# Performance work log

Hardware: AMD Instinct MI355X
Metric: run time of the kernel (lower is better)

Reference implementation:

```python
import jax, jax.numpy as jnp
import numpy as np

B, T, DIN, DC, CS = 8, 4096, 1024, 256, 8192
EPS = 1e-12

def _l2norm(x):
    # F.normalize: x / max(||x||_2, eps) along last axis
    n = jnp.sqrt(jnp.sum(x * x, axis=-1, keepdims=True))
    return x / jnp.maximum(n, EPS)

def _wn(v, g):
    # torch weight_norm(dim=0): w = g * v / ||v|| per output row
    n = jnp.sqrt(jnp.sum(v * v, axis=1, keepdims=True))
    return g * v / jnp.maximum(n, EPS)

def setup_inputs() -> dict:
    key = jax.random.key(0)
    k = jax.random.split(key, 4)
    return {
        "z": jax.random.normal(k[0], (B, DIN, T), jnp.float32),
        "in_v": jax.random.normal(k[1], (DC, DIN), jnp.float32) * 0.02,
        "in_g": jnp.ones((DC, 1), jnp.float32),
        "in_b": jnp.zeros((DC,), jnp.float32),
        "out_v": jax.random.normal(k[2], (DIN, DC), jnp.float32) * 0.02,
        "out_g": jnp.ones((DIN, 1), jnp.float32),
        "out_b": jnp.zeros((DIN,), jnp.float32),
        "codebook": jax.random.normal(k[3], (CS, DC), jnp.float32),
    }

def reference(z, in_v, in_g, in_b, out_v, out_g, out_b, codebook):
    b, _, t = z.shape
    w_in = _wn(in_v, in_g)                      # (DC, DIN)
    z_e = jnp.einsum('bdt,cd->bct', z, w_in) + in_b[None, :, None]  # (B, DC, T)

    # decode_latents (eval mode: dropout p=0)
    enc = _l2norm(z_e.transpose(0, 2, 1).reshape(b * t, -1))   # (BT, DC)
    cb = _l2norm(codebook)                                     # (CS, DC)
    dist = (jnp.sum(enc * enc, axis=1, keepdims=True)
            - 2.0 * enc @ cb.T
            + jnp.sum(cb * cb, axis=1)[None, :])               # (BT, CS)
    indices = jnp.argmax(-dist, axis=1).reshape(b, t)          # (B, T)
    z_q = codebook[indices].transpose(0, 2, 1)                 # (B, DC, T)

    commitment_loss = jnp.mean((z_e - jax.lax.stop_gradient(z_q)) ** 2, axis=(1, 2))
    codebook_loss = jnp.mean((z_q - jax.lax.stop_gradient(z_e)) ** 2, axis=(1, 2))

    z_q_st = z_e + jax.lax.stop_gradient(z_q - z_e)            # straight-through
    w_out = _wn(out_v, out_g)                                  # (DIN, DC)
    z_q_out = jnp.einsum('bct,dc->bdt', z_q_st, w_out) + out_b[None, :, None]
    return (z_q_out, commitment_loss, codebook_loss, indices)
```

## Files before the change

### kernel.cpp

```cpp
#include <hip/hip_runtime.h>
#include <stdint.h>

#define BB 8
#define TT 4096
#define DIN 1024
#define DC 256
#define CS 8192
#define EPSF 1e-12f

typedef unsigned short ushort_t;
typedef __attribute__((ext_vector_type(8))) short short8;
typedef __attribute__((ext_vector_type(4))) float f32x4;

constexpr size_t OFF_WIN   = 0;
constexpr size_t OFF_WOUTT = OFF_WIN   + 1048576;
constexpr size_t OFF_CBN   = OFF_WOUTT + 1048576;
constexpr size_t OFF_NRM2  = OFF_CBN   + 8388608;
constexpr size_t OFF_ZE    = OFF_NRM2  + 32768;
constexpr size_t OFF_INV   = OFF_ZE    + 33554432;
constexpr size_t OFF_ENC2  = OFF_INV   + 131072;
constexpr size_t OFF_KEYS  = OFF_ENC2  + 131072;
constexpr size_t OFF_LOSS  = OFF_KEYS  + 262144;
constexpr size_t OFF_WSPL  = OFF_LOSS  + 256;
constexpr size_t OFF_W2T   = OFF_WSPL  + 1048576;
constexpr size_t REQ_WS_ZE = OFF_W2T + 134217728ull;

__device__ __forceinline__ float block_reduce_sum_256(float v, float* sbuf) {
  #pragma unroll
  for (int o = 32; o > 0; o >>= 1) v += __shfl_down(v, o, 64);
  int lane = threadIdx.x & 63, w = threadIdx.x >> 6;
  if (lane == 0) sbuf[w] = v;
  __syncthreads();
  float r = sbuf[0] + sbuf[1] + sbuf[2] + sbuf[3];
  __syncthreads();
  return r;
}

__device__ __forceinline__ ushort_t bf16_rne(float x) {
  unsigned u = __float_as_uint(x);
  unsigned r = (u + 0x7FFFu + ((u >> 16) & 1u)) >> 16;
  return (ushort_t)r;
}
__device__ __forceinline__ float bf16f(ushort_t h) {
  return __uint_as_float(((unsigned)h) << 16);
}

__device__ __forceinline__ int swz4(int r) {
  return (r + (r >> 2)) & 3;
}

__device__ __forceinline__ void async_copy16(const ushort_t* g, ushort_t* lds) {
  __builtin_amdgcn_global_load_lds(
      (const __attribute__((address_space(1))) void*)g,
      (__attribute__((address_space(3))) void*)lds, 16, 0, 0);
}

__device__ __forceinline__ void stage_tile8(const ushort_t* __restrict__ s0,
                                            ushort_t* __restrict__ dstbuf,
                                            const int (&go)[8]) {
  #pragma unroll
  for (int i = 0; i < 8; i++) async_copy16(s0 + go[i], dstbuf + i*512);
}

__device__ __forceinline__ void stage2(const ushort_t* __restrict__ srcbase,
                                       ushort_t* __restrict__ comp,
                                       const int (&go)[2], int wu) {
  async_copy16(srcbase + go[0], comp + wu);
  async_copy16(srcbase + go[1], comp + wu + 4096);
}

#define LD8(base, off) (*(const short8*)((const char*)(base) + (off)))

template<int MH, int CLO>
__device__ __forceinline__ void qmfma(f32x4 (&acc)[8][4],
    const short8 (&fah)[4], const short8 (&fal)[4],
    const short8 (&fbh)[4], const short8 (&fbl)[4]) {
  #pragma unroll
  for (int r = 0; r < 4; r++) {
    #pragma unroll
    for (int c2 = 0; c2 < 2; c2++) {
      f32x4 t = acc[MH*4 + r][CLO + c2];
      t = __builtin_amdgcn_mfma_f32_16x16x32_bf16(fah[r], fbh[CLO + c2], t, 0, 0, 0);
      t = __builtin_amdgcn_mfma_f32_16x16x32_bf16(fal[r], fbh[CLO + c2], t, 0, 0, 0);
      t = __builtin_amdgcn_mfma_f32_16x16x32_bf16(fah[r], fbl[CLO + c2], t, 0, 0, 0);
      acc[MH*4 + r][CLO + c2] = t;
    }
  }
}

__global__ void k_prep_win(const float* __restrict__ v, const float* __restrict__ g,
                           float* __restrict__ w, ushort_t* __restrict__ wh,
                           ushort_t* __restrict__ wl) {
  __shared__ float sb[4];
  int r = blockIdx.x, t = threadIdx.x;
  float xv[4]; float s = 0.f;
  #pragma unroll
  for (int i = 0; i < 4; i++) { xv[i] = v[r*DIN + t + i*256]; s += xv[i]*xv[i]; }
  s = block_reduce_sum_256(s, sb);
  float sc = g[r] / fmaxf(sqrtf(s), EPSF);
  #pragma unroll
  for (int i = 0; i < 4; i++) {
    float val = xv[i] * sc;
    int idx = r*DIN + t + i*256;
    w[idx] = val;
    ushort_t h = bf16_rne(val);
    wh[idx] = h;
    wl[idx] = bf16_rne(val - bf16f(h));
  }
}

__global__ void k_prep_wout(const float* __restrict__ v, const float* __restrict__ g,
                            float* __restrict__ wT) {
  __shared__ float sb[4];
  int r = blockIdx.x, t = threadIdx.x;
  float x = v[r*DC + t];
  float s = block_reduce_sum_256(x*x, sb);
  float sc = g[r] / fmaxf(sqrtf(s), EPSF);
  wT[t*DIN + r] = x * sc;
}

__global__ void k_prep_cb(const float* __restrict__ cb, ushort_t* __restrict__ cbh,
                          ushort_t* __restrict__ cbl, float* __restrict__ nrm2) {
  __shared__ float sb[4];
  int j = blockIdx.x, t = threadIdx.x;
  float x = cb[j*DC + t];
  float s = block_reduce_sum_256(x*x, sb);
  float nm = fmaxf(sqrtf(s), EPSF);
  float cn = x / nm;
  ushort_t h = bf16_rne(cn);
  cbh[j*DC + t] = h;
  cbl[j*DC + t] = bf16_rne(cn - bf16f(h));
  float q = block_reduce_sum_256(cn*cn, sb);
  if (t == 0) nrm2[j] = q;
}

__global__ void k_split_cbraw(const float* __restrict__ cb, ushort_t* __restrict__ ch,
                              ushort_t* __restrict__ cl) {
  int j = blockIdx.x, t = threadIdx.x;
  float x = cb[j*DC + t];
  ushort_t h = bf16_rne(x);
  ch[j*DC + t] = h;
  cl[j*DC + t] = bf16_rne(x - bf16f(h));
}

__global__ void k_split_wout(const float* __restrict__ v, const float* __restrict__ g,
                             ushort_t* __restrict__ wh, ushort_t* __restrict__ wl) {
  __shared__ float sb[4];
  int r = blockIdx.x, t = threadIdx.x;
  float x = v[r*DC + t];
  float s = block_reduce_sum_256(x*x, sb);
  float sc = g[r] / fmaxf(sqrtf(s), EPSF);
  float val = x * sc;
  ushort_t h = bf16_rne(val);
  wh[r*DC + t] = h;
  wl[r*DC + t] = bf16_rne(val - bf16f(h));
}

template<bool BIAS>
__global__ __launch_bounds__(256) void k_gemm(
    const float* __restrict__ A, const float* __restrict__ Bmat,
    const float* __restrict__ bias, float* __restrict__ C,
    int K, int lda, int ldb, int ldc, size_t strideB, size_t strideC)
{
  __shared__ float As[16][132];
  __shared__ float Bs[16][132];
  const int bn = blockIdx.x * 128;
  const int bm = blockIdx.y * 128;
  const float* Bb = Bmat + (size_t)blockIdx.z * strideB;
  float* Cb = C + (size_t)blockIdx.z * strideC;
  const int tid = threadIdx.x;
  const int tx = tid & 15, ty = tid >> 4;
  const int am = tid & 127, akq = (tid >> 7) * 8;
  const int bk = tid >> 5, bj = (tid & 31) * 4;

  float acc[8][8];
  #pragma unroll
  for (int i = 0; i < 8; i++)
    #pragma unroll
    for (int j = 0; j < 8; j++) acc[i][j] = 0.f;

  for (int k0 = 0; k0 < K; k0 += 16) {
    float4 a0 = *(const float4*)&A[(size_t)(bm+am)*lda + k0 + akq];
    float4 a1 = *(const float4*)&A[(size_t)(bm+am)*lda + k0 + akq + 4];
    float4 b0 = *(const float4*)&Bb[(size_t)(k0+bk)*ldb + bn + bj];
    float4 b1 = *(const float4*)&Bb[(size_t)(k0+bk+8)*ldb + bn + bj];
    As[akq+0][am] = a0.x; As[akq+1][am] = a0.y; As[akq+2][am] = a0.z; As[akq+3][am] = a0.w;
    As[akq+4][am] = a1.x; As[akq+5][am] = a1.y; As[akq+6][am] = a1.z; As[akq+7][am] = a1.w;
    *(float4*)&Bs[bk][bj] = b0;
    *(float4*)&Bs[bk+8][bj] = b1;
    __syncthreads();
    #pragma unroll
    for (int k = 0; k < 16; k++) {
      float av[8], bv[8];
      float4 x0 = *(const float4*)&As[k][tx*4];
      float4 x1 = *(const float4*)&As[k][tx*4+64];
      float4 y0 = *(const float4*)&Bs[k][ty*4];
      float4 y1 = *(const float4*)&Bs[k][ty*4+64];
      av[0]=x0.x; av[1]=x0.y; av[2]=x0.z; av[3]=x0.w;
      av[4]=x1.x; av[5]=x1.y; av[6]=x1.z; av[7]=x1.w;
      bv[0]=y0.x; bv[1]=y0.y; bv[2]=y0.z; bv[3]=y0.w;
      bv[4]=y1.x; bv[5]=y1.y; bv[6]=y1.z; bv[7]=y1.w;
      #pragma unroll
      for (int i = 0; i < 8; i++)
        #pragma unroll
        for (int j = 0; j < 8; j++)
          acc[i][j] += av[i] * bv[j];
    }
    __syncthreads();
  }

  #pragma unroll
  for (int i = 0; i < 8; i++) {
    int mm = bm + ((i < 4) ? tx*4 + i : 64 + tx*4 + (i-4));
    float bia = BIAS ? bias[mm] : 0.f;
    float4 v0 = make_float4(acc[i][0]+bia, acc[i][1]+bia, acc[i][2]+bia, acc[i][3]+bia);
    float4 v1 = make_float4(acc[i][4]+bia, acc[i][5]+bia, acc[i][6]+bia, acc[i][7]+bia);
    *(float4*)&Cb[(size_t)mm*ldc + bn + ty*4]      = v0;
    *(float4*)&Cb[(size_t)mm*ldc + bn + 64 + ty*4] = v1;
  }
}

__global__ void k_split_z(const float* __restrict__ z, ushort_t* __restrict__ zhi,
                          ushort_t* __restrict__ zlo) {
  __shared__ float tile[64][65];
  int b = blockIdx.z, t0 = blockIdx.x * 64, d0 = blockIdx.y * 64;
  int tx = threadIdx.x & 63, ty = threadIdx.x >> 6;
  const float* zb = z + (size_t)b*DIN*TT;
  #pragma unroll
  for (int i = 0; i < 16; i++) {
    int d = i*4 + ty;
    tile[d][tx] = zb[(size_t)(d0+d)*TT + t0 + tx];
  }
  __syncthreads();
  #pragma unroll
  for (int i = 0; i < 16; i++) {
    int t = i*4 + ty;
    float val = tile[tx][t];
    ushort_t h = bf16_rne(val);
    size_t o = ((size_t)(b*TT + t0 + t))*DIN + d0 + tx;
    zhi[o] = h;
    zlo[o] = bf16_rne(val - bf16f(h));
  }
}

__global__ __launch_bounds__(256) void k_ze_mfma(
    const ushort_t* __restrict__ zth, const ushort_t* __restrict__ ztl,
    const ushort_t* __restrict__ wh, const ushort_t* __restrict__ wl,
    const float* __restrict__ in_b, float* __restrict__ ze)
{
  __shared__ ushort_t As_hi[2][4096];
  __shared__ ushort_t As_lo[2][4096];
  __shared__ ushort_t Bs_hi[2][4096];
  __shared__ ushort_t Bs_lo[2][4096];

  const int b  = blockIdx.z;
  const int t0 = blockIdx.x * 128;
  const int c0 = blockIdx.y * 128;
  const int tid = threadIdx.x;
  const int lane = tid & 63;
  const int wave = tid >> 6;
  const int wr = wave >> 1, wc = wave & 1;
  const int m = lane & 15, quad = lane >> 4;

  const ushort_t* src; ushort_t* dst;
  {
    size_t aoff = ((size_t)(b*TT + t0)) * DIN;
    size_t boff = (size_t)c0 * DIN;
    if      (wave == 0) { src = zth + aoff; dst = &As_hi[0][0]; }
    else if (wave == 1) { src = ztl + aoff; dst = &As_lo[0][0]; }
    else if (wave == 2) { src = wh + boff;  dst = &Bs_hi[0][0]; }
    else                { src = wl + boff;  dst = &Bs_lo[0][0]; }
  }
  const int rr = lane >> 2, cc = lane & 3;

  int goT[8];
  #pragma unroll
  for (int i = 0; i < 8; i++) {
    int r = i*16 + rr;
    int g = cc ^ swz4(r);
    goT[i] = r*DIN + (g << 3);
  }

  int offA[4], offB[4];
  #pragma unroll
  for (int ri = 0; ri < 4; ri++) {
    int r = wr*64 + ri*16 + m;
    int p = quad ^ swz4(r);
    offA[ri] = r*64 + p*16;
  }
  #pragma unroll
  for (int ci = 0; ci < 4; ci++) {
    int r = wc*64 + ci*16 + m;
    int p = quad ^ swz4(r);
    offB[ci] = r*64 + p*16;
  }

  f32x4 acc[4][4];
  #pragma unroll
  for (int i = 0; i < 4; i++)
    #pragma unroll
    for (int j = 0; j < 4; j++) acc[i][j] = (f32x4)0.f;

  stage_tile8(src, dst, goT);

  for (int it = 0; it < 32; ++it) {
    __syncthreads();
    if (it < 31) stage_tile8(src + (it+1)*32, dst + ((it+1)&1)*4096, goT);
    const int bo = (it & 1) << 13;

    short8 bh[4], bl[4];
    #pragma unroll
    for (int ci = 0; ci < 4; ci++) {
      bh[ci] = *(const short8*)((const char*)Bs_hi + bo + offB[ci]);
      bl[ci] = *(const short8*)((const char*)Bs_lo + bo + offB[ci]);
    }
    #pragma unroll
    for (int ri = 0; ri < 4; ri++) {
      short8 ah = *(const short8*)((const char*)As_hi + bo + offA[ri]);
      short8 al = *(const short8*)((const char*)As_lo + bo + offA[ri]);
      #pragma unroll
      for (int ci = 0; ci < 4; ci++) {
        acc[ri][ci] = __builtin_amdgcn_mfma_f32_16x16x32_bf16(ah, bh[ci], acc[ri][ci], 0, 0, 0);
        acc[ri][ci] = __builtin_amdgcn_mfma_f32_16x16x32_bf16(al, bh[ci], acc[ri][ci], 0, 0, 0);
        acc[ri][ci] = __builtin_amdgcn_mfma_f32_16x16x32_bf16(ah, bl[ci], acc[ri][ci], 0, 0, 0);
      }
    }
  }

  #pragma unroll
  for (int ri = 0; ri < 4; ri++) {
    int t_loc = wr*64 + ri*16 + quad*4;
    #pragma unroll
    for (int ci = 0; ci < 4; ci++) {
      int c_loc = wc*64 + ci*16 + m;
      float bia = in_b[c0 + c_loc];
      float4 v = make_float4(acc[ri][ci][0]+bia, acc[ri][ci][1]+bia,
                             acc[ri][ci][2]+bia, acc[ri][ci][3]+bia);
      *(float4*)&ze[((size_t)b*DC + c0 + c_loc)*TT + t0 + t_loc] = v;
    }
  }
}

__global__ __launch_bounds__(256) void k_w2t_mfma(
    const ushort_t* __restrict__ ah_g, const ushort_t* __restrict__ al_g,
    const ushort_t* __restrict__ bh_g, const ushort_t* __restrict__ bl_g,
    float* __restrict__ C)
{
  __shared__ ushort_t As_hi[2][4096];
  __shared__ ushort_t As_lo[2][4096];
  __shared__ ushort_t Bs_hi[2][4096];
  __shared__ ushort_t Bs_lo[2][4096];

  const int m0 = blockIdx.x * 128;
  const int n0 = blockIdx.y * 128;
  const int tid = threadIdx.x;
  const int lane = tid & 63;
  const int wave = tid >> 6;
  const int wr = wave >> 1, wc = wave & 1;
  const int m = lane & 15, quad = lane >> 4;

  const ushort_t* src; ushort_t* dst;
  {
    size_t aoff = (size_t)m0 * DC;
    size_t boff = (size_t)n0 * DC;
    if      (wave == 0) { src = ah_g + aoff; dst = &As_hi[0][0]; }
    else if (wave == 1) { src = al_g + aoff; dst = &As_lo[0][0]; }
    else if (wave == 2) { src = bh_g + boff; dst = &Bs_hi[0][0]; }
    else                { src = bl_g + boff; dst = &Bs_lo[0][0]; }
  }
  const int rr = lane >> 2, cc = lane & 3;

  int goT[8];
  #pragma unroll
  for (int i = 0; i < 8; i++) {
    int r = i*16 + rr;
    int g = cc ^ swz4(r);
    goT[i] = r*DC + (g << 3);
  }

  int offA[4], offB[4];
  #pragma unroll
  for (int ri = 0; ri < 4; ri++) {
    int r = wr*64 + ri*16 + m;
    int p = quad ^ swz4(r);
    offA[ri] = r*64 + p*16;
  }
  #pragma unroll
  for (int ci = 0; ci < 4; ci++) {
    int r = wc*64 + ci*16 + m;
    int p = quad ^ swz4(r);
    offB[ci] = r*64 + p*16;
  }

  f32x4 acc[4][4];
  #pragma unroll
  for (int i = 0; i < 4; i++)
    #pragma unroll
    for (int j = 0; j < 4; j++) acc[i][j] = (f32x4)0.f;

  stage_tile8(src, dst, goT);

  for (int it = 0; it < 8; ++it) {
    __syncthreads();
    if (it < 7) stage_tile8(src + (it+1)*32, dst + ((it+1)&1)*4096, goT);
    const int bo = (it & 1) << 13;

    short8 bh[4], bl[4];
    #pragma unroll
    for (int ci = 0; ci < 4; ci++) {
      bh[ci] = *(const short8*)((const char*)Bs_hi + bo + offB[ci]);
      bl[ci] = *(const short8*)((const char*)Bs_lo + bo + offB[ci]);
    }
    #pragma unroll
    for (int ri = 0; ri < 4; ri++) {
      short8 ah = *(const short8*)((const char*)As_hi + bo + offA[ri]);
      short8 al = *(const short8*)((const char*)As_lo + bo + offA[ri]);
      #pragma unroll
      for (int ci = 0; ci < 4; ci++) {
        acc[ri][ci] = __builtin_amdgcn_mfma_f32_16x16x32_bf16(ah, bh[ci], acc[ri][ci], 0, 0, 0);
        acc[ri][ci] = __builtin_amdgcn_mfma_f32_16x16x32_bf16(al, bh[ci], acc[ri][ci], 0, 0, 0);
        acc[ri][ci] = __builtin_amdgcn_mfma_f32_16x16x32_bf16(ah, bl[ci], acc[ri][ci], 0, 0, 0);
      }
    }
  }

  #pragma unroll
  for (int ri = 0; ri < 4; ri++) {
    int m_loc = wr*64 + ri*16 + quad*4;
    #pragma unroll
    for (int ci = 0; ci < 4; ci++) {
      int n_loc = wc*64 + ci*16 + m;
      #pragma unroll
      for (int reg = 0; reg < 4; reg++) {
        C[(size_t)(m0 + m_loc + reg)*DIN + n0 + n_loc] = acc[ri][ci][reg];
      }
    }
  }
}

__global__ void k_colnorm(const float* __restrict__ ze, float* __restrict__ inv,
                          float* __restrict__ enc2) {
  int r = blockIdx.x * 256 + threadIdx.x;
  int b = r >> 12, t = r & 4095;
  const float* p = ze + (size_t)b*DC*TT + t;
  float s = 0.f;
  for (int c = 0; c < DC; c++) { float x = p[(size_t)c*TT]; s += x*x; }
  float iv = 1.f / fmaxf(sqrtf(s), EPSF);
  inv[r] = iv;
  enc2[r] = (s * iv) * iv;
}

__global__ void k_split_enc(const float* __restrict__ ze, const float* __restrict__ inv,
                            ushort_t* __restrict__ ehi, ushort_t* __restrict__ elo) {
  __shared__ float tile[64][65];
  int b = blockIdx.z, t0 = blockIdx.x * 64, c0 = blockIdx.y * 64;
  int tx = threadIdx.x & 63, ty = threadIdx.x >> 6;
  const float* zb = ze + (size_t)b*DC*TT;
  #pragma unroll
  for (int i = 0; i < 16; i++) {
    int c = i*4 + ty;
    tile[c][tx] = zb[(size_t)(c0+c)*TT + t0 + tx];
  }
  __syncthreads();
  #pragma unroll
  for (int i = 0; i < 16; i++) {
    int t = i*4 + ty;
    float iv = inv[b*TT + t0 + t];
    float val = tile[tx][t] * iv;
    ushort_t h = bf16_rne(val);
    size_t o = ((size_t)(b*TT + t0 + t))*DC + c0 + tx;
    ehi[o] = h;
    elo[o] = bf16_rne(val - bf16f(h));
  }
}

__global__ __launch_bounds__(512, 2) void k_dist_mfma(
    const ushort_t* __restrict__ ehi, const ushort_t* __restrict__ elo,
    const ushort_t* __restrict__ cbh, const ushort_t* __restrict__ cbl,
    const float* __restrict__ nrm2, const float* __restrict__ enc2,
    unsigned long long* __restrict__ keys)
{
  __shared__ ushort_t sAh[2][8192];
  __shared__ ushort_t sAl[2][8192];
  __shared__ ushort_t sBh[2][8192];
  __shared__ ushort_t sBl[2][8192];
  __shared__ float sE2[256], sN2[256];
  __shared__ unsigned long long rkey[256];

  const int j0 = blockIdx.x * 256;
  const size_t r0 = (size_t)blockIdx.y * 256;
  const int tid = threadIdx.x;
  const int lane = tid & 63;
  const int wave = tid >> 6;
  const int wr = wave >> 2, wc = wave & 3;
  const int ml = lane & 15, quad = lane >> 4;

  if (tid < 256) {
    sE2[tid] = enc2[r0 + tid];
    sN2[tid] = nrm2[j0 + tid];
    rkey[tid] = 0xFFFFFFFFFFFFFFFFull;
  }

  const ushort_t* gAh = ehi + r0 * DC;
  const ushort_t* gAl = elo + r0 * DC;
  const ushort_t* gBh = cbh + (size_t)j0 * DC;
  const ushort_t* gBl = cbl + (size_t)j0 * DC;

  int goS[2];
  #pragma unroll
  for (int l = 0; l < 2; l++) {
    int chunk = l*512 + tid;
    int r = chunk >> 2, c = chunk & 3;
    int g = c ^ swz4(r);
    goS[l] = r*DC + (g << 3);
  }
  const int wu = wave * 512;

  int offA[8], offB[4];
  #pragma unroll
  for (int i = 0; i < 8; i++) {
    int r = wr*128 + i*16 + ml;
    int p = quad ^ swz4(r);
    offA[i] = r*64 + p*16;
  }
  #pragma unroll
  for (int i = 0; i < 4; i++) {
    int r = wc*64 + i*16 + ml;
    int p = quad ^ swz4(r);
    offB[i] = r*64 + p*16;
  }

  f32x4 acc[8][4];
  #pragma unroll
  for (int i = 0; i < 8; i++)
    #pragma unroll
    for (int j = 0; j < 4; j++) acc[i][j] = (f32x4)0.f;

  stage2(gBh,      &sBh[0][0], goS, wu);
  stage2(gBl,      &sBl[0][0], goS, wu);
  stage2(gAh,      &sAh[0][0], goS, wu);
  stage2(gAl,      &sAl[0][0], goS, wu);
  stage2(gBh + 32, &sBh[1][0], goS, wu);
  stage2(gBl + 32, &sBl[1][0], goS, wu);
  asm volatile("s_waitcnt vmcnt(4)" ::: "memory");
  asm volatile("s_waitcnt lgkmcnt(0)" ::: "memory");
  __builtin_amdgcn_s_barrier();
  __builtin_amdgcn_sched_barrier(0);

  short8 fa_h[4], fa_l[4], fb_h[4], fb_l[4];

  #pragma unroll 2
  for (int k = 0; k < 8; k++) {
    const int cb = k & 1, nb = cb ^ 1;
    const char* pAh = (const char*)&sAh[cb][0];
    const char* pAl = (const char*)&sAl[cb][0];
    const char* pBh = (const char*)&sBh[cb][0];
    const char* pBl = (const char*)&sBl[cb][0];
    __builtin_amdgcn_sched_barrier(0);

    #pragma unroll
    for (int i = 0; i < 4; i++) { fa_h[i] = LD8(pAh, offA[i]); fa_l[i] = LD8(pAl, offA[i]); }
    #pragma unroll
    for (int i = 0; i < 2; i++) { fb_h[i] = LD8(pBh, offB[i]); fb_l[i] = LD8(pBl, offB[i]); }
    if (k < 7) stage2(gAh + (size_t)(k+1)*32, &sAh[nb][0], goS, wu);
    __builtin_amdgcn_s_barrier();
    __builtin_amdgcn_s_setprio(1);
    qmfma<0, 0>(acc, fa_h, fa_l, fb_h, fb_l);
    __builtin_amdgcn_s_setprio(0);
    __builtin_amdgcn_s_barrier();

    #pragma unroll
    for (int i = 2; i < 4; i++) { fb_h[i] = LD8(pBh, offB[i]); fb_l[i] = LD8(pBl, offB[i]); }
    if (k < 7) stage2(gAl + (size_t)(k+1)*32, &sAl[nb][0], goS, wu);
    __builtin_amdgcn_s_barrier();
    __builtin_amdgcn_s_setprio(1);
    qmfma<0, 2>(acc, fa_h, fa_l, fb_h, fb_l);
    __builtin_amdgcn_s_setprio(0);
    __builtin_amdgcn_s_barrier();

    #pragma unroll
    for (int i = 0; i < 4; i++) { fa_h[i] = LD8(pAh, offA[4+i]); fa_l[i] = LD8(pAl, offA[4+i]); }
    if (k < 6) {
      stage2(gBh + (size_t)(k+2)*32, &sBh[cb][0], goS, wu);
      stage2(gBl + (size_t)(k+2)*32, &sBl[cb][0], goS, wu);
    }
    __builtin_amdgcn_s_barrier();
    __builtin_amdgcn_s_setprio(1);
    qmfma<1, 2>(acc, fa_h, fa_l, fb_h, fb_l);
    qmfma<1, 0>(acc, fa_h, fa_l, fb_h, fb_l);
    __builtin_amdgcn_s_setprio(0);
    if (k < 6) { asm volatile("s_waitcnt vmcnt(4)" ::: "memory"); }
    else       { asm volatile("s_waitcnt vmcnt(0)" ::: "memory"); }
    __builtin_amdgcn_s_barrier();
  }

  #pragma unroll
  for (int ri = 0; ri < 8; ri++) {
    #pragma unroll
    for (int reg = 0; reg < 4; reg++) {
      int t_loc = wr*128 + ri*16 + quad*4 + reg;
      float e2 = sE2[t_loc];
      unsigned long long best = 0xFFFFFFFFFFFFFFFFull;
      #pragma unroll
      for (int ci = 0; ci < 4; ci++) {
        int j_loc = wc*64 + ci*16 + ml;
        float d = e2 - 2.0f * acc[ri][ci][reg];
        d = d + sN2[j_loc];
        unsigned long long key =
            ((unsigned long long)__float_as_uint(d) << 32) | (unsigned)(j0 + j_loc);
        best = key < best ? key : best;
      }
      #pragma unroll
      for (int off = 1; off < 16; off <<= 1) {
        unsigned long long o = __shfl_xor(best, off);
        best = o < best ? o : best;
      }
      if (ml == 0) atomicMin(&rkey[t_loc], best);
    }
  }
  __syncthreads();
  if (tid < 256) atomicMin(&keys[r0 + tid], rkey[tid]);
}

__global__ void k_lossidx(const float* __restrict__ ze, const float* __restrict__ cb,
                          const unsigned long long* __restrict__ keys,
                          float* __restrict__ loss_sums, float* __restrict__ out_idx)
{
  __shared__ float sb[4];
  __shared__ int sj[64];
  int b = blockIdx.y, t0 = blockIdx.x * 64;
  int tid = threadIdx.x;
  if (tid < 64) {
    unsigned long long k = keys[(size_t)b*TT + t0 + tid];
    int j = (int)(unsigned)(k & 0xFFFFFFFFull);
    sj[tid] = j;
    out_idx[(size_t)b*TT + t0 + tid] = (float)j;
  }
  __syncthreads();
  int tt = tid & 63, tc = tid >> 6;
  const float* zb = ze + (size_t)b*DC*TT + t0;
  int j = sj[tt];
  float s = 0.f;
  for (int ci = 0; ci < 64; ci++) {
    int c = tc + ci*4;
    float zev = zb[(size_t)c*TT + tt];
    float zqv = cb[(size_t)j*DC + c];
    float d = zev - zqv;
    s += d*d;
  }
  s = block_reduce_sum_256(s, sb);
  if (tid == 0) atomicAdd(&loss_sums[b], s);
}

__global__ void k_losswrite(const float* __restrict__ loss_sums, float* __restrict__ out_loss) {
  int i = threadIdx.x;
  if (i < 8) {
    float v = loss_sums[i] * (1.f/1048576.f);
    out_loss[i] = v;
    out_loss[8 + i] = v;
  }
}

__global__ void k_outgather(const float* __restrict__ W2T,
                            const unsigned long long* __restrict__ keys,
                            const float* __restrict__ out_b, float* __restrict__ out)
{
  __shared__ float tile[64][65];
  __shared__ int sj[64];
  int b = blockIdx.y, t0 = blockIdx.x * 64;
  int tid = threadIdx.x;
  if (tid < 64) sj[tid] = (int)(unsigned)(keys[(size_t)b*TT + t0 + tid] & 0xFFFFFFFFull);
  __syncthreads();
  float* ob = out + (size_t)b*DIN*TT;
  int dd = tid & 63, tq = tid >> 6;
  for (int d0 = 0; d0 < DIN; d0 += 64) {
    #pragma unroll
    for (int i = 0; i < 16; i++) {
      int t = tq*16 + i;
      tile[t][dd] = W2T[(size_t)sj[t]*DIN + d0 + dd];
    }
    __syncthreads();
    #pragma unroll
    for (int i = 0; i < 16; i++) {
      int d = tq*16 + i;
      ob[(size_t)(d0+d)*TT + t0 + dd] = tile[dd][d] + out_b[d0+d];
    }
    __syncthreads();
  }
}

extern "C" void kernel_launch(void* const* d_in, const int* in_sizes, int n_in,
                              void* d_out, int out_size, void* d_ws, size_t ws_size,
                              hipStream_t stream) {
  const float* z        = (const float*)d_in[0];
  const float* in_v     = (const float*)d_in[1];
  const float* in_g     = (const float*)d_in[2];
  const float* in_b     = (const float*)d_in[3];
  const float* out_v    = (const float*)d_in[4];
  const float* out_g    = (const float*)d_in[5];
  const float* out_b    = (const float*)d_in[6];
  const float* codebook = (const float*)d_in[7];

  char* w = (char*)d_ws;
  float* w_in   = (float*)(w + OFF_WIN);
  float* w_outT = (float*)(w + OFF_WOUTT);
  ushort_t* cb_hi = (ushort_t*)(w + OFF_CBN);
  ushort_t* cb_lo = cb_hi + (size_t)CS*DC;
  float* nrm2   = (float*)(w + OFF_NRM2);
  float* z_e    = (float*)(w + OFF_ZE);
  float* inv    = (float*)(w + OFF_INV);
  float* enc2   = (float*)(w + OFF_ENC2);
  unsigned long long* keys = (unsigned long long*)(w + OFF_KEYS);
  float* loss_sums = (float*)(w + OFF_LOSS);
  ushort_t* w_hi = (ushort_t*)(w + OFF_WSPL);
  ushort_t* w_lo = w_hi + (size_t)DC*DIN;
  ushort_t* zt_hi = (ushort_t*)(w + OFF_W2T);
  ushort_t* zt_lo = zt_hi + (size_t)BB*TT*DIN;
  ushort_t* enc_hi = (ushort_t*)(w + OFF_W2T);
  ushort_t* enc_lo = enc_hi + (size_t)BB*TT*DC;
  float* W2T    = (float*)(w + OFF_W2T);
  ushort_t* cbr_hi  = (ushort_t*)(w + OFF_W2T + 33554432);
  ushort_t* cbr_lo  = cbr_hi + (size_t)CS*DC;
  ushort_t* wout_hi = (ushort_t*)(w + OFF_W2T + 33554432 + 8388608);
  ushort_t* wout_lo = wout_hi + (size_t)DIN*DC;

  float* out      = (float*)d_out;
  float* out_loss = out + (size_t)BB*DIN*TT;
  float* out_idx  = out_loss + 16;

  hipMemsetAsync(keys, 0xFF, 32768ull*8, stream);
  hipMemsetAsync(loss_sums, 0, 32, stream);

  const bool mfma_path = (ws_size >= REQ_WS_ZE);

  k_prep_win <<<256, 256, 0, stream>>>(in_v, in_g, w_in, w_hi, w_lo);
  k_prep_cb  <<<8192, 256, 0, stream>>>(codebook, cb_hi, cb_lo, nrm2);

  if (mfma_path) {
    k_split_z<<<dim3(64, 16, 8), 256, 0, stream>>>(z, zt_hi, zt_lo);
    k_ze_mfma<<<dim3(32, 2, 8), 256, 0, stream>>>(zt_hi, zt_lo, w_hi, w_lo, in_b, z_e);
  } else {
    k_prep_wout<<<1024, 256, 0, stream>>>(out_v, out_g, w_outT);
    k_gemm<true><<<dim3(32, 2, 8), 256, 0, stream>>>(
        w_in, z, in_b, z_e, 1024, 1024, 4096, 4096,
        (size_t)DIN*TT, (size_t)DC*TT);
  }

  k_colnorm<<<128, 256, 0, stream>>>(z_e, inv, enc2);
  k_split_enc<<<dim3(64, 4, 8), 256, 0, stream>>>(z_e, inv, enc_hi, enc_lo);

  k_dist_mfma<<<dim3(32, 128), 512, 0, stream>>>(
      enc_hi, enc_lo, cb_hi, cb_lo, nrm2, enc2, keys);

  k_lossidx<<<dim3(64, 8), 256, 0, stream>>>(z_e, codebook, keys, loss_sums, out_idx);
  k_losswrite<<<1, 64, 0, stream>>>(loss_sums, out_loss);

  if (mfma_path) {
    k_split_cbraw<<<8192, 256, 0, stream>>>(codebook, cbr_hi, cbr_lo);
    k_split_wout <<<1024, 256, 0, stream>>>(out_v, out_g, wout_hi, wout_lo);
    k_w2t_mfma<<<dim3(64, 8), 256, 0, stream>>>(cbr_hi, cbr_lo, wout_hi, wout_lo, W2T);
  } else {
    k_gemm<false><<<dim3(8, 64, 1), 256, 0, stream>>>(
        codebook, w_outT, nullptr, W2T, 256, 256, 1024, 1024,
        (size_t)0, (size_t)0);
  }

  k_outgather<<<dim3(64, 8), 256, 0, stream>>>(W2T, keys, out_b, out);
}
```

Baseline: 907.7 us.

## Fuse z_e GEMM with row normalization and bf16 split, reconstruct losses algebraically

The z_e projection kernel now computes a full 256-channel row tile per block (512 threads), adds the bias, reduces squared norms in-block, and writes the normalized hi/lo bf16 encodings, inverse norms and enc2 directly. This skips materializing fp32 z_e and drops the separate colnorm and split_enc passes. The commitment and codebook losses are rebuilt from the chosen distance key using the raw codebook and encoder norms, so the gather-based loss kernel is no longer needed. In exchange the loss carries extra rounding from the bf16-split distance, and the larger tile needs more shared memory and registers per block.

Result: faster. 877.8 us (-3.3%).

```diff
diff --git a/kernel.cpp b/kernel.cpp
--- a/kernel.cpp
+++ b/kernel.cpp
@@ -120,7 +120,8 @@
 }
 
 __global__ void k_prep_cb(const float* __restrict__ cb, ushort_t* __restrict__ cbh,
-                          ushort_t* __restrict__ cbl, float* __restrict__ nrm2) {
+                          ushort_t* __restrict__ cbl, float* __restrict__ nrm2,
+                          float* __restrict__ nmraw, float* __restrict__ n2raw) {
   __shared__ float sb[4];
   int j = blockIdx.x, t = threadIdx.x;
   float x = cb[j*DC + t];
@@ -131,7 +132,7 @@
   cbh[j*DC + t] = h;
   cbl[j*DC + t] = bf16_rne(cn - bf16f(h));
   float q = block_reduce_sum_256(cn*cn, sb);
-  if (t == 0) nrm2[j] = q;
+  if (t == 0) { nrm2[j] = q; nmraw[j] = nm; n2raw[j] = s; }
 }
 
 __global__ void k_split_cbraw(const float* __restrict__ cb, ushort_t* __restrict__ ch,
@@ -243,56 +244,58 @@
   }
 }
 
-__global__ __launch_bounds__(256) void k_ze_mfma(
+__global__ __launch_bounds__(512) void k_ze_enc(
     const ushort_t* __restrict__ zth, const ushort_t* __restrict__ ztl,
     const ushort_t* __restrict__ wh, const ushort_t* __restrict__ wl,
-    const float* __restrict__ in_b, float* __restrict__ ze)
+    const float* __restrict__ in_b,
+    ushort_t* __restrict__ ehi, ushort_t* __restrict__ elo,
+    float* __restrict__ inv, float* __restrict__ enc2, float* __restrict__ e2raw)
 {
-  __shared__ ushort_t As_hi[2][4096];
-  __shared__ ushort_t As_lo[2][4096];
-  __shared__ ushort_t Bs_hi[2][4096];
-  __shared__ ushort_t Bs_lo[2][4096];
-
-  const int b  = blockIdx.z;
+  __shared__ ushort_t smem[49152];
+  __shared__ float e2s[128][4];
+  __shared__ float sIv[128];
+
+  ushort_t* sAh = smem;
+  ushort_t* sAl = smem + 8192;
+  ushort_t* sBh = smem + 16384;
+  ushort_t* sBl = smem + 32768;
+
   const int t0 = blockIdx.x * 128;
-  const int c0 = blockIdx.y * 128;
+  const int b  = blockIdx.y;
   const int tid = threadIdx.x;
   const int lane = tid & 63;
   const int wave = tid >> 6;
-  const int wr = wave >> 1, wc = wave & 1;
-  const int m = lane & 15, quad = lane >> 4;
-
-  const ushort_t* src; ushort_t* dst;
-  {
-    size_t aoff = ((size_t)(b*TT + t0)) * DIN;
-    size_t boff = (size_t)c0 * DIN;
-    if      (wave == 0) { src = zth + aoff; dst = &As_hi[0][0]; }
-    else if (wave == 1) { src = ztl + aoff; dst = &As_lo[0][0]; }
-    else if (wave == 2) { src = wh + boff;  dst = &Bs_hi[0][0]; }
-    else                { src = wl + boff;  dst = &Bs_lo[0][0]; }
-  }
-  const int rr = lane >> 2, cc = lane & 3;
-
-  int goT[8];
-  #pragma unroll
-  for (int i = 0; i < 8; i++) {
-    int r = i*16 + rr;
-    int g = cc ^ swz4(r);
-    goT[i] = r*DIN + (g << 3);
-  }
+  const int wr = wave >> 2, wc = wave & 3;
+  const int ml = lane & 15, quad = lane >> 4;
+  const size_t r0 = (size_t)b*TT + t0;
+
+  const ushort_t* gAh = zth + r0*DIN;
+  const ushort_t* gAl = ztl + r0*DIN;
+
+  int goA;
+  { int r = tid >> 2, c = tid & 3; int g = c ^ swz4(r); goA = r*DIN + (g << 3); }
+  int goB[2];
+  #pragma unroll
+  for (int l = 0; l < 2; l++) {
+    int chunk = l*512 + tid;
+    int r = chunk >> 2, c = chunk & 3;
+    int g = c ^ swz4(r);
+    goB[l] = r*DIN + (g << 3);
+  }
+  const int wu = wave * 512;
 
   int offA[4], offB[4];
   #pragma unroll
-  for (int ri = 0; ri < 4; ri++) {
-    int r = wr*64 + ri*16 + m;
+  for (int i = 0; i < 4; i++) {
+    int r = wr*64 + i*16 + ml;
     int p = quad ^ swz4(r);
-    offA[ri] = r*64 + p*16;
-  }
-  #pragma unroll
-  for (int ci = 0; ci < 4; ci++) {
-    int r = wc*64 + ci*16 + m;
+    offA[i] = r*64 + p*16;
+  }
+  #pragma unroll
+  for (int i = 0; i < 4; i++) {
+    int r = wc*64 + i*16 + ml;
     int p = quad ^ swz4(r);
-    offB[ci] = r*64 + p*16;
+    offB[i] = r*64 + p*16;
   }
 
   f32x4 acc[4][4];
@@ -301,43 +304,116 @@
     #pragma unroll
     for (int j = 0; j < 4; j++) acc[i][j] = (f32x4)0.f;
 
-  stage_tile8(src, dst, goT);
+  async_copy16(gAh + goA, sAh + wu);
+  async_copy16(gAl + goA, sAl + wu);
+  stage2(wh, sBh, goB, wu);
+  stage2(wl, sBl, goB, wu);
 
   for (int it = 0; it < 32; ++it) {
     __syncthreads();
-    if (it < 31) stage_tile8(src + (it+1)*32, dst + ((it+1)&1)*4096, goT);
-    const int bo = (it & 1) << 13;
-
-    short8 bh[4], bl[4];
+    if (it < 31) {
+      const int nb = (it+1) & 1;
+      async_copy16(gAh + goA + (it+1)*32, sAh + nb*4096 + wu);
+      async_copy16(gAl + goA + (it+1)*32, sAl + nb*4096 + wu);
+      stage2(wh + (it+1)*32, sBh + nb*8192, goB, wu);
+      stage2(wl + (it+1)*32, sBl + nb*8192, goB, wu);
+    }
+    const char* pAh = (const char*)(sAh + (it & 1)*4096);
+    const char* pAl = (const char*)(sAl + (it & 1)*4096);
+    const char* pBh = (const char*)(sBh + (it & 1)*8192);
+    const char* pBl = (const char*)(sBl + (it & 1)*8192);
+
+    short8 fbh[4], fbl[4];
     #pragma unroll
     for (int ci = 0; ci < 4; ci++) {
-      bh[ci] = *(const short8*)((const char*)Bs_hi + bo + offB[ci]);
-      bl[ci] = *(const short8*)((const char*)Bs_lo + bo + offB[ci]);
+      fbh[ci] = LD8(pBh, offB[ci]);
+      fbl[ci] = LD8(pBl, offB[ci]);
     }
     #pragma unroll
     for (int ri = 0; ri < 4; ri++) {
-      short8 ah = *(const short8*)((const char*)As_hi + bo + offA[ri]);
-      short8 al = *(const short8*)((const char*)As_lo + bo + offA[ri]);
+      short8 ah = LD8(pAh, offA[ri]);
+      short8 al = LD8(pAl, offA[ri]);
       #pragma unroll
       for (int ci = 0; ci < 4; ci++) {
-        acc[ri][ci] = __builtin_amdgcn_mfma_f32_16x16x32_bf16(ah, bh[ci], acc[ri][ci], 0, 0, 0);
-        acc[ri][ci] = __builtin_amdgcn_mfma_f32_16x16x32_bf16(al, bh[ci], acc[ri][ci], 0, 0, 0);
-        acc[ri][ci] = __builtin_amdgcn_mfma_f32_16x16x32_bf16(ah, bl[ci], acc[ri][ci], 0, 0, 0);
+        acc[ri][ci] = __builtin_amdgcn_mfma_f32_16x16x32_bf16(ah, fbh[ci], acc[ri][ci], 0, 0, 0);
+        acc[ri][ci] = __builtin_amdgcn_mfma_f32_16x16x32_bf16(al, fbh[ci], acc[ri][ci], 0, 0, 0);
+        acc[ri][ci] = __builtin_amdgcn_mfma_f32_16x16x32_bf16(ah, fbl[ci], acc[ri][ci], 0, 0, 0);
       }
     }
   }
 
+  float bia[4];
+  #pragma unroll
+  for (int ci = 0; ci < 4; ci++) bia[ci] = in_b[wc*64 + ci*16 + ml];
+
   #pragma unroll
   for (int ri = 0; ri < 4; ri++) {
-    int t_loc = wr*64 + ri*16 + quad*4;
-    #pragma unroll
-    for (int ci = 0; ci < 4; ci++) {
-      int c_loc = wc*64 + ci*16 + m;
-      float bia = in_b[c0 + c_loc];
-      float4 v = make_float4(acc[ri][ci][0]+bia, acc[ri][ci][1]+bia,
-                             acc[ri][ci][2]+bia, acc[ri][ci][3]+bia);
-      *(float4*)&ze[((size_t)b*DC + c0 + c_loc)*TT + t0 + t_loc] = v;
-    }
+    #pragma unroll
+    for (int reg = 0; reg < 4; reg++) {
+      float p = 0.f;
+      #pragma unroll
+      for (int ci = 0; ci < 4; ci++) {
+        float v = acc[ri][ci][reg] + bia[ci];
+        acc[ri][ci][reg] = v;
+        p += v*v;
+      }
+      #pragma unroll
+      for (int off = 1; off < 16; off <<= 1) p += __shfl_xor(p, off);
+      if (ml == 0) e2s[wr*64 + ri*16 + quad*4 + reg][wc] = p;
+    }
+  }
+  __syncthreads();
+  if (tid < 128) {
+    float s = ((e2s[tid][0] + e2s[tid][1]) + e2s[tid][2]) + e2s[tid][3];
+    float iv = 1.f / fmaxf(sqrtf(s), EPSF);
+    sIv[tid] = iv;
+    inv[r0 + tid]   = iv;
+    enc2[r0 + tid]  = (s * iv) * iv;
+    e2raw[r0 + tid] = s;
+  }
+  __syncthreads();
+
+  ushort_t* tb = smem;
+  #pragma unroll
+  for (int ri = 0; ri < 4; ri++) {
+    #pragma unroll
+    for (int reg = 0; reg < 4; reg++) {
+      int t_loc = wr*64 + ri*16 + quad*4 + reg;
+      float ivt = sIv[t_loc];
+      #pragma unroll
+      for (int ci = 0; ci < 4; ci++) {
+        int c_loc = wc*64 + ci*16 + ml;
+        tb[t_loc*256 + c_loc] = bf16_rne(acc[ri][ci][reg] * ivt);
+      }
+    }
+  }
+  __syncthreads();
+  #pragma unroll
+  for (int p = 0; p < 8; p++) {
+    int ch = p*512 + tid;
+    *(short8*)(ehi + r0*DC + (size_t)ch*8) = *(const short8*)(tb + ch*8);
+  }
+  __syncthreads();
+  #pragma unroll
+  for (int ri = 0; ri < 4; ri++) {
+    #pragma unroll
+    for (int reg = 0; reg < 4; reg++) {
+      int t_loc = wr*64 + ri*16 + quad*4 + reg;
+      float ivt = sIv[t_loc];
+      #pragma unroll
+      for (int ci = 0; ci < 4; ci++) {
+        int c_loc = wc*64 + ci*16 + ml;
+        float v = acc[ri][ci][reg] * ivt;
+        ushort_t h = bf16_rne(v);
+        tb[t_loc*256 + c_loc] = bf16_rne(v - bf16f(h));
+      }
+    }
+  }
+  __syncthreads();
+  #pragma unroll
+  for (int p = 0; p < 8; p++) {
+    int ch = p*512 + tid;
+    *(short8*)(elo + r0*DC + (size_t)ch*8) = *(const short8*)(tb + ch*8);
   }
 }
 
@@ -440,7 +516,7 @@
 
 __global__ void k_colnorm(const float* __restrict__ ze, float* __restrict__ inv,
                           float* __restrict__ enc2) {
-  int r = blockIdx.x * 256 + threadIdx.x;
+  int r = blockIdx.x * 128 + threadIdx.x;
   int b = r >> 12, t = r & 4095;
   const float* p = ze + (size_t)b*DC*TT + t;
   float s = 0.f;
@@ -472,154 +548,6 @@
     ehi[o] = h;
     elo[o] = bf16_rne(val - bf16f(h));
   }
-}
-
-__global__ __launch_bounds__(512, 2) void k_dist_mfma(
-    const ushort_t* __restrict__ ehi, const ushort_t* __restrict__ elo,
-    const ushort_t* __restrict__ cbh, const ushort_t* __restrict__ cbl,
-    const float* __restrict__ nrm2, const float* __restrict__ enc2,
-    unsigned long long* __restrict__ keys)
-{
-  __shared__ ushort_t sAh[2][8192];
-  __shared__ ushort_t sAl[2][8192];
-  __shared__ ushort_t sBh[2][8192];
-  __shared__ ushort_t sBl[2][8192];
-  __shared__ float sE2[256], sN2[256];
-  __shared__ unsigned long long rkey[256];
-
-  const int j0 = blockIdx.x * 256;
-  const size_t r0 = (size_t)blockIdx.y * 256;
-  const int tid = threadIdx.x;
-  const int lane = tid & 63;
-  const int wave = tid >> 6;
-  const int wr = wave >> 2, wc = wave & 3;
-  const int ml = lane & 15, quad = lane >> 4;
-
-  if (tid < 256) {
-    sE2[tid] = enc2[r0 + tid];
-    sN2[tid] = nrm2[j0 + tid];
-    rkey[tid] = 0xFFFFFFFFFFFFFFFFull;
-  }
-
-  const ushort_t* gAh = ehi + r0 * DC;
-  const ushort_t* gAl = elo + r0 * DC;
-  const ushort_t* gBh = cbh + (size_t)j0 * DC;
-  const ushort_t* gBl = cbl + (size_t)j0 * DC;
-
-  int goS[2];
-  #pragma unroll
-  for (int l = 0; l < 2; l++) {
-    int chunk = l*512 + tid;
-    int r = chunk >> 2, c = chunk & 3;
-    int g = c ^ swz4(r);
-    goS[l] = r*DC + (g << 3);
-  }
-  const int wu = wave * 512;
-
-  int offA[8], offB[4];
-  #pragma unroll
-  for (int i = 0; i < 8; i++) {
-    int r = wr*128 + i*16 + ml;
-    int p = quad ^ swz4(r);
-    offA[i] = r*64 + p*16;
-  }
-  #pragma unroll
-  for (int i = 0; i < 4; i++) {
-    int r = wc*64 + i*16 + ml;
-    int p = quad ^ swz4(r);
-    offB[i] = r*64 + p*16;
-  }
-
-  f32x4 acc[8][4];
-  #pragma unroll
-  for (int i = 0; i < 8; i++)
-    #pragma unroll
-    for (int j = 0; j < 4; j++) acc[i][j] = (f32x4)0.f;
-
-  stage2(gBh,      &sBh[0][0], goS, wu);
-  stage2(gBl,      &sBl[0][0], goS, wu);
-  stage2(gAh,      &sAh[0][0], goS, wu);
-  stage2(gAl,      &sAl[0][0], goS, wu);
-  stage2(gBh + 32, &sBh[1][0], goS, wu);
-  stage2(gBl + 32, &sBl[1][0], goS, wu);
-  asm volatile("s_waitcnt vmcnt(4)" ::: "memory");
-  asm volatile("s_waitcnt lgkmcnt(0)" ::: "memory");
-  __builtin_amdgcn_s_barrier();
-  __builtin_amdgcn_sched_barrier(0);
-
-  short8 fa_h[4], fa_l[4], fb_h[4], fb_l[4];
-
-  #pragma unroll 2
-  for (int k = 0; k < 8; k++) {
-    const int cb = k & 1, nb = cb ^ 1;
-    const char* pAh = (const char*)&sAh[cb][0];
-    const char* pAl = (const char*)&sAl[cb][0];
-    const char* pBh = (const char*)&sBh[cb][0];
-    const char* pBl = (const char*)&sBl[cb][0];
-    __builtin_amdgcn_sched_barrier(0);
-
-    #pragma unroll
-    for (int i = 0; i < 4; i++) { fa_h[i] = LD8(pAh, offA[i]); fa_l[i] = LD8(pAl, offA[i]); }
-    #pragma unroll
-    for (int i = 0; i < 2; i++) { fb_h[i] = LD8(pBh, offB[i]); fb_l[i] = LD8(pBl, offB[i]); }
-    if (k < 7) stage2(gAh + (size_t)(k+1)*32, &sAh[nb][0], goS, wu);
-    __builtin_amdgcn_s_barrier();
-    __builtin_amdgcn_s_setprio(1);
-    qmfma<0, 0>(acc, fa_h, fa_l, fb_h, fb_l);
-    __builtin_amdgcn_s_setprio(0);
-    __builtin_amdgcn_s_barrier();
-
-    #pragma unroll
-    for (int i = 2; i < 4; i++) { fb_h[i] = LD8(pBh, offB[i]); fb_l[i] = LD8(pBl, offB[i]); }
-    if (k < 7) stage2(gAl + (size_t)(k+1)*32, &sAl[nb][0], goS, wu);
-    __builtin_amdgcn_s_barrier();
-    __builtin_amdgcn_s_setprio(1);
-    qmfma<0, 2>(acc, fa_h, fa_l, fb_h, fb_l);
-    __builtin_amdgcn_s_setprio(0);
-    __builtin_amdgcn_s_barrier();
-
-    #pragma unroll
-    for (int i = 0; i < 4; i++) { fa_h[i] = LD8(pAh, offA[4+i]); fa_l[i] = LD8(pAl, offA[4+i]); }
-    if (k < 6) {
-      stage2(gBh + (size_t)(k+2)*32, &sBh[cb][0], goS, wu);
-      stage2(gBl + (size_t)(k+2)*32, &sBl[cb][0], goS, wu);
-    }
-    __builtin_amdgcn_s_barrier();
-    __builtin_amdgcn_s_setprio(1);
-    qmfma<1, 2>(acc, fa_h, fa_l, fb_h, fb_l);
-    qmfma<1, 0>(acc, fa_h, fa_l, fb_h, fb_l);
-    __builtin_amdgcn_s_setprio(0);
-    if (k < 6) { asm volatile("s_waitcnt vmcnt(4)" ::: "memory"); }
-    else       { asm volatile("s_waitcnt vmcnt(0)" ::: "memory"); }
-    __builtin_amdgcn_s_barrier();
-  }
-
-  #pragma unroll
-  for (int ri = 0; ri < 8; ri++) {
-    #pragma unroll
-    for (int reg = 0; reg < 4; reg++) {
-      int t_loc = wr*128 + ri*16 + quad*4 + reg;
-      float e2 = sE2[t_loc];
-      unsigned long long best = 0xFFFFFFFFFFFFFFFFull;
-      #pragma unroll
-      for (int ci = 0; ci < 4; ci++) {
-        int j_loc = wc*64 + ci*16 + ml;
-        float d = e2 - 2.0f * acc[ri][ci][reg];
-        d = d + sN2[j_loc];
-        unsigned long long key =
-            ((unsigned long long)__float_as_uint(d) << 32) | (unsigned)(j0 + j_loc);
-        best = key < best ? key : best;
-      }
-      #pragma unroll
-      for (int off = 1; off < 16; off <<= 1) {
-        unsigned long long o = __shfl_xor(best, off);
-        best = o < best ? o : best;
-      }
-      if (ml == 0) atomicMin(&rkey[t_loc], best);
-    }
-  }
-  __syncthreads();
-  if (tid < 256) atomicMin(&keys[r0 + tid], rkey[tid]);
 }
 
 __global__ void k_lossidx(const float* __restrict__ ze, const float* __restrict__ cb,
@@ -652,6 +580,174 @@
   if (tid == 0) atomicAdd(&loss_sums[b], s);
 }
 
+__global__ __launch_bounds__(512, 2) void k_dist_mfma(
+    const ushort_t* __restrict__ ehi, const ushort_t* __restrict__ elo,
+    const ushort_t* __restrict__ cbh, const ushort_t* __restrict__ cbl,
+    const float* __restrict__ nrm2, const float* __restrict__ enc2,
+    unsigned long long* __restrict__ keys)
+{
+  __shared__ ushort_t sAh[2][8192];
+  __shared__ ushort_t sAl[2][8192];
+  __shared__ ushort_t sBh[2][8192];
+  __shared__ ushort_t sBl[2][8192];
+  __shared__ float sE2[256], sN2[256];
+  __shared__ unsigned long long rkey[256];
+
+  const int j0 = blockIdx.x * 256;
+  const size_t r0 = (size_t)blockIdx.y * 256;
+  const int tid = threadIdx.x;
+  const int lane = tid & 63;
+  const int wave = tid >> 6;
+  const int wr = wave >> 2, wc = wave & 3;
+  const int ml = lane & 15, quad = lane >> 4;
+
+  if (tid < 256) {
+    sE2[tid] = enc2[r0 + tid];
+    sN2[tid] = nrm2[j0 + tid];
+    rkey[tid] = 0xFFFFFFFFFFFFFFFFull;
+  }
+
+  const ushort_t* gAh = ehi + r0 * DC;
+  const ushort_t* gAl = elo + r0 * DC;
+  const ushort_t* gBh = cbh + (size_t)j0 * DC;
+  const ushort_t* gBl = cbl + (size_t)j0 * DC;
+
+  int goS[2];
+  #pragma unroll
+  for (int l = 0; l < 2; l++) {
+    int chunk = l*512 + tid;
+    int r = chunk >> 2, c = chunk & 3;
+    int g = c ^ swz4(r);
+    goS[l] = r*DC + (g << 3);
+  }
+  const int wu = wave * 512;
+
+  int offA[8], offB[4];
+  #pragma unroll
+  for (int i = 0; i < 8; i++) {
+    int r = wr*128 + i*16 + ml;
+    int p = quad ^ swz4(r);
+    offA[i] = r*64 + p*16;
+  }
+  #pragma unroll
+  for (int i = 0; i < 4; i++) {
+    int r = wc*64 + i*16 + ml;
+    int p = quad ^ swz4(r);
+    offB[i] = r*64 + p*16;
+  }
+
+  f32x4 acc[8][4];
+  #pragma unroll
+  for (int i = 0; i < 8; i++)
+    #pragma unroll
+    for (int j = 0; j < 4; j++) acc[i][j] = (f32x4)0.f;
+
+  stage2(gBh,      &sBh[0][0], goS, wu);
+  stage2(gBl,      &sBl[0][0], goS, wu);
+  stage2(gAh,      &sAh[0][0], goS, wu);
+  stage2(gAl,      &sAl[0][0], goS, wu);
+  stage2(gBh + 32, &sBh[1][0], goS, wu);
+  stage2(gBl + 32, &sBl[1][0], goS, wu);
+  asm volatile("s_waitcnt vmcnt(4)" ::: "memory");
+  asm volatile("s_waitcnt lgkmcnt(0)" ::: "memory");
+  __builtin_amdgcn_s_barrier();
+  __builtin_amdgcn_sched_barrier(0);
+
+  short8 fa_h[4], fa_l[4], fb_h[4], fb_l[4];
+
+  #pragma unroll 2
+  for (int k = 0; k < 8; k++) {
+    const int cb = k & 1, nb = cb ^ 1;
+    const char* pAh = (const char*)&sAh[cb][0];
+    const char* pAl = (const char*)&sAl[cb][0];
+    const char* pBh = (const char*)&sBh[cb][0];
+    const char* pBl = (const char*)&sBl[cb][0];
+    __builtin_amdgcn_sched_barrier(0);
+
+    #pragma unroll
+    for (int i = 0; i < 4; i++) { fa_h[i] = LD8(pAh, offA[i]); fa_l[i] = LD8(pAl, offA[i]); }
+    #pragma unroll
+    for (int i = 0; i < 2; i++) { fb_h[i] = LD8(pBh, offB[i]); fb_l[i] = LD8(pBl, offB[i]); }
+    if (k < 7) stage2(gAh + (size_t)(k+1)*32, &sAh[nb][0], goS, wu);
+    __builtin_amdgcn_s_barrier();
+    __builtin_amdgcn_s_setprio(1);
+    qmfma<0, 0>(acc, fa_h, fa_l, fb_h, fb_l);
+    __builtin_amdgcn_s_setprio(0);
+    __builtin_amdgcn_s_barrier();
+
+    #pragma unroll
+    for (int i = 2; i < 4; i++) { fb_h[i] = LD8(pBh, offB[i]); fb_l[i] = LD8(pBl, offB[i]); }
+    if (k < 7) stage2(gAl + (size_t)(k+1)*32, &sAl[nb][0], goS, wu);
+    __builtin_amdgcn_s_barrier();
+    __builtin_amdgcn_s_setprio(1);
+    qmfma<0, 2>(acc, fa_h, fa_l, fb_h, fb_l);
+    __builtin_amdgcn_s_setprio(0);
+    __builtin_amdgcn_s_barrier();
+
+    #pragma unroll
+    for (int i = 0; i < 4; i++) { fa_h[i] = LD8(pAh, offA[4+i]); fa_l[i] = LD8(pAl, offA[4+i]); }
+    if (k < 6) {
+      stage2(gBh + (size_t)(k+2)*32, &sBh[cb][0], goS, wu);
+      stage2(gBl + (size_t)(k+2)*32, &sBl[cb][0], goS, wu);
+    }
+    __builtin_amdgcn_s_barrier();
+    __builtin_amdgcn_s_setprio(1);
+    qmfma<1, 2>(acc, fa_h, fa_l, fb_h, fb_l);
+    qmfma<1, 0>(acc, fa_h, fa_l, fb_h, fb_l);
+    __builtin_amdgcn_s_setprio(0);
+    if (k < 6) { asm volatile("s_waitcnt vmcnt(4)" ::: "memory"); }
+    else       { asm volatile("s_waitcnt vmcnt(0)" ::: "memory"); }
+    __builtin_amdgcn_s_barrier();
+  }
+
+  #pragma unroll
+  for (int ri = 0; ri < 8; ri++) {
+    #pragma unroll
+    for (int reg = 0; reg < 4; reg++) {
+      int t_loc = wr*128 + ri*16 + quad*4 + reg;
+      float e2 = sE2[t_loc];
+      unsigned long long best = 0xFFFFFFFFFFFFFFFFull;
+      #pragma unroll
+      for (int ci = 0; ci < 4; ci++) {
+        int j_loc = wc*64 + ci*16 + ml;
+        float d = e2 - 2.0f * acc[ri][ci][reg];
+        d = d + sN2[j_loc];
+        unsigned long long key =
+            ((unsigned long long)__float_as_uint(d) << 32) | (unsigned)(j0 + j_loc);
+        best = key < best ? key : best;
+      }
+      #pragma unroll
+      for (int off = 1; off < 16; off <<= 1) {
+        unsigned long long o = __shfl_xor(best, off);
+        best = o < best ? o : best;
+      }
+      if (ml == 0) atomicMin(&rkey[t_loc], best);
+    }
+  }
+  __syncthreads();
+  if (tid < 256) atomicMin(&keys[r0 + tid], rkey[tid]);
+}
+
+__global__ void k_lossrec(const unsigned long long* __restrict__ keys,
+                          const float* __restrict__ enc2, const float* __restrict__ nrm2,
+                          const float* __restrict__ e2raw, const float* __restrict__ inv,
+                          const float* __restrict__ nmraw, const float* __restrict__ n2raw,
+                          float* __restrict__ loss_sums, float* __restrict__ out_idx)
+{
+  __shared__ float sb[4];
+  int r = blockIdx.x * 256 + threadIdx.x;
+  int b = r >> 12;
+  unsigned long long k = keys[r];
+  int j = (int)(unsigned)(k & 0xFFFFFFFFull);
+  float d = __uint_as_float((unsigned)(k >> 32));
+  out_idx[r] = (float)j;
+  float dotn = 0.5f * (enc2[r] + nrm2[j] - d);
+  float dot_raw = nmraw[j] * dotn / inv[r];
+  float le = e2raw[r] - 2.f*dot_raw + n2raw[j];
+  float s = block_reduce_sum_256(le, sb);
+  if (threadIdx.x == 0) atomicAdd(&loss_sums[b], s);
+}
+
 __global__ void k_losswrite(const float* __restrict__ loss_sums, float* __restrict__ out_loss) {
   int i = threadIdx.x;
   if (i < 8) {
@@ -704,10 +800,15 @@
   char* w = (char*)d_ws;
   float* w_in   = (float*)(w + OFF_WIN);
   float* w_outT = (float*)(w + OFF_WOUTT);
+  float* e2raw  = (float*)(w + OFF_WOUTT);
+  float* nmraw  = (float*)(w + OFF_WOUTT + 131072);
+  float* n2raw  = (float*)(w + OFF_WOUTT + 163840);
   ushort_t* cb_hi = (ushort_t*)(w + OFF_CBN);
   ushort_t* cb_lo = cb_hi + (size_t)CS*DC;
   float* nrm2   = (float*)(w + OFF_NRM2);
   float* z_e    = (float*)(w + OFF_ZE);
+  ushort_t* enc_hi_m = (ushort_t*)(w + OFF_ZE);
+  ushort_t* enc_lo_m = enc_hi_m + (size_t)BB*TT*DC;
   float* inv    = (float*)(w + OFF_INV);
   float* enc2   = (float*)(w + OFF_ENC2);
   unsigned long long* keys = (unsigned long long*)(w + OFF_KEYS);
@@ -716,8 +817,8 @@
   ushort_t* w_lo = w_hi + (size_t)DC*DIN;
   ushort_t* zt_hi = (ushort_t*)(w + OFF_W2T);
   ushort_t* zt_lo = zt_hi + (size_t)BB*TT*DIN;
-  ushort_t* enc_hi = (ushort_t*)(w + OFF_W2T);
-  ushort_t* enc_lo = enc_hi + (size_t)BB*TT*DC;
+  ushort_t* enc_hi_fb = (ushort_t*)(w + OFF_W2T);
+  ushort_t* enc_lo_fb = enc_hi_fb + (size_t)BB*TT*DC;
   float* W2T    = (float*)(w + OFF_W2T);
   ushort_t* cbr_hi  = (ushort_t*)(w + OFF_W2T + 33554432);
   ushort_t* cbr_lo  = cbr_hi + (size_t)CS*DC;
@@ -734,32 +835,37 @@
   const bool mfma_path = (ws_size >= REQ_WS_ZE);
 
   k_prep_win <<<256, 256, 0, stream>>>(in_v, in_g, w_in, w_hi, w_lo);
-  k_prep_cb  <<<8192, 256, 0, stream>>>(codebook, cb_hi, cb_lo, nrm2);
+  k_prep_cb  <<<8192, 256, 0, stream>>>(codebook, cb_hi, cb_lo, nrm2, nmraw, n2raw);
 
   if (mfma_path) {
     k_split_z<<<dim3(64, 16, 8), 256, 0, stream>>>(z, zt_hi, zt_lo);
-    k_ze_mfma<<<dim3(32, 2, 8), 256, 0, stream>>>(zt_hi, zt_lo, w_hi, w_lo, in_b, z_e);
+    k_ze_enc<<<dim3(32, 8), 512, 0, stream>>>(
+        zt_hi, zt_lo, w_hi, w_lo, in_b, enc_hi_m, enc_lo_m, inv, enc2, e2raw);
+
+    k_dist_mfma<<<dim3(32, 128), 512, 0, stream>>>(
+        enc_hi_m, enc_lo_m, cb_hi, cb_lo, nrm2, enc2, keys);
+
+    k_lossrec<<<128, 256, 0, stream>>>(
+        keys, enc2, nrm2, e2raw, inv, nmraw, n2raw, loss_sums, out_idx);
+    k_losswrite<<<1, 64, 0, stream>>>(loss_sums, out_loss);
+
+    k_split_cbraw<<<8192, 256, 0, stream>>>(codebook, cbr_hi, cbr_lo);
+    k_split_wout <<<1024, 256, 0, stream>>>(out_v, out_g, wout_hi, wout_lo);
+    k_w2t_mfma<<<dim3(64, 8), 256, 0, stream>>>(cbr_hi, cbr_lo, wout_hi, wout_lo, W2T);
   } else {
     k_prep_wout<<<1024, 256, 0, stream>>>(out_v, out_g, w_outT);
     k_gemm<true><<<dim3(32, 2, 8), 256, 0, stream>>>(
         w_in, z, in_b, z_e, 1024, 1024, 4096, 4096,
         (size_t)DIN*TT, (size_t)DC*TT);
-  }
-
-  k_colnorm<<<128, 256, 0, stream>>>(z_e, inv, enc2);
-  k_split_enc<<<dim3(64, 4, 8), 256, 0, stream>>>(z_e, inv, enc_hi, enc_lo);
-
-  k_dist_mfma<<<dim3(32, 128), 512, 0, stream>>>(
-      enc_hi, enc_lo, cb_hi, cb_lo, nrm2, enc2, keys);
-
-  k_lossidx<<<dim3(64, 8), 256, 0, stream>>>(z_e, codebook, keys, loss_sums, out_idx);
-  k_losswrite<<<1, 64, 0, stream>>>(loss_sums, out_loss);
-
-  if (mfma_path) {
-    k_split_cbraw<<<8192, 256, 0, stream>>>(codebook, cbr_hi, cbr_lo);
-    k_split_wout <<<1024, 256, 0, stream>>>(out_v, out_g, wout_hi, wout_lo);
-    k_w2t_mfma<<<dim3(64, 8), 256, 0, stream>>>(cbr_hi, cbr_lo, wout_hi, wout_lo, W2T);
-  } else {
+    k_colnorm<<<256, 128, 0, stream>>>(z_e, inv, enc2);
+    k_split_enc<<<dim3(64, 4, 8), 256, 0, stream>>>(z_e, inv, enc_hi_fb, enc_lo_fb);
+
+    k_dist_mfma<<<dim3(32, 128), 512, 0, stream>>>(
+        enc_hi_fb, enc_lo_fb, cb_hi, cb_lo, nrm2, enc2, keys);
+
+    k_lossidx<<<dim3(64, 8), 256, 0, stream>>>(z_e, codebook, keys, loss_sums, out_idx);
+    k_losswrite<<<1, 64, 0, stream>>>(loss_sums, out_loss);
+
     k_gemm<false><<<dim3(8, 64, 1), 256, 0, stream>>>(
         codebook, w_outT, nullptr, W2T, 256, 256, 1024, 1024,
         (size_t)0, (size_t)0);
```
